# Performance work log

Hardware: AMD Instinct MI355X
Metric: run time of the kernel (lower is better)

The kernel has to match this reference:

```python
import jax, jax.numpy as jnp
import numpy as np

B, T_ENC, T_DEC = 64, 100, 50
L = 512      # lstm_size
E = 512      # input_encoding_size
H = 512      # att_hidden_size
R = 8        # num_review_steps
V_TOK = 30001  # token_cnt + 1 embedding rows
V_OUT = 30000  # word_cnt


def _lstm_maxout(s, c):
    # ARNet/neuraltalk2 LSTMCore: 5*L preactivations, maxout input transform
    i = jax.nn.sigmoid(s[:, :L])
    f = jax.nn.sigmoid(s[:, L:2 * L])
    o = jax.nn.sigmoid(s[:, 2 * L:3 * L])
    t = jnp.maximum(s[:, 3 * L:4 * L], s[:, 4 * L:])
    c2 = f * c + i * t
    return o * jnp.tanh(c2), c2


def _attend(feats, h, Wa2a, ba2a, Wh2a, bh2a, Watt, batt):
    # feats: [B, A, F], h: [B, L] -> context [B, F]
    p = jnp.tanh(feats @ Wa2a + ba2a + (h @ Wh2a + bh2a)[:, None, :])  # [B,A,H]
    e = jnp.squeeze(p @ Watt, -1) + batt                               # [B,A]
    a = jax.nn.softmax(e, axis=-1)
    return jnp.einsum('ba,baf->bf', a, feats)


def setup_inputs() -> dict:
    key = jax.random.key(0)
    ks = iter(jax.random.split(key, 48))
    g = lambda shape: jax.random.normal(next(ks), shape, jnp.float32) * 0.05
    z = lambda shape: jnp.zeros(shape, jnp.float32)
    return {
        'code_matrix': jax.random.randint(next(ks), (B, T_ENC), 0, V_TOK),
        'comment_matrix': jax.random.randint(next(ks), (B, T_DEC), 0, V_TOK),
        'current_comment_mask_cuda': jnp.ones((B, T_DEC), jnp.float32),
        'embed': jax.random.uniform(next(ks), (V_TOK, E), jnp.float32, -0.1, 0.1),
        'enc_Wi': g((E, 5 * L)), 'enc_bi': z((5 * L,)),
        'enc_Wh': g((L, 5 * L)), 'enc_bh': z((5 * L,)),
        'rev_Wh': g((R, L, 5 * L)), 'rev_bh': z((R, 5 * L)),
        'rev_Wa': g((R, L, 5 * L)), 'rev_ba': z((R, 5 * L)),
        'rev_Wa2a': g((R, L, H)), 'rev_ba2a': z((R, H)),
        'rev_Wh2a': g((R, L, H)), 'rev_bh2a': z((R, H)),
        'rev_Watt': g((R, H, 1)), 'rev_batt': z((R,)),
        'dec_Wi': g((E, 5 * L)), 'dec_bi': z((5 * L,)),
        'dec_Wh': g((L, 5 * L)), 'dec_bh': z((5 * L,)),
        'dec_Wa': g((L, 5 * L)), 'dec_ba': z((5 * L,)),
        'dec_Wa2a': g((L, H)), 'dec_ba2a': z((H,)),
        'dec_Wh2a': g((L, H)), 'dec_bh2a': z((H,)),
        'dec_Watt': g((H, 1)), 'dec_batt': z(()),
        'logit_W': jax.random.uniform(next(ks), (L, V_OUT), jnp.float32, -0.1, 0.1),
        'logit_b': z((V_OUT,)),
    }


def reference(code_matrix, comment_matrix, current_comment_mask_cuda, embed,
              enc_Wi, enc_bi, enc_Wh, enc_bh,
              rev_Wh, rev_bh, rev_Wa, rev_ba, rev_Wa2a, rev_ba2a,
              rev_Wh2a, rev_bh2a, rev_Watt, rev_batt,
              dec_Wi, dec_bi, dec_Wh, dec_bh, dec_Wa, dec_ba,
              dec_Wa2a, dec_ba2a, dec_Wh2a, dec_bh2a, dec_Watt, dec_batt,
              logit_W, logit_b):
    del current_comment_mask_cuda  # only used by scheduled sampling (ss_prob=0)
    Bsz = code_matrix.shape[0]
    h0 = jnp.zeros((Bsz, L), embed.dtype)
    c0 = jnp.zeros((Bsz, L), embed.dtype)

    # ---- encode ----
    enc_x = embed[code_matrix]  # [B, T_enc, E]

    def enc_step(carry, xt):
        h, c = carry
        s = xt @ enc_Wi + enc_bi + h @ enc_Wh + enc_bh
        h2, c2 = _lstm_maxout(s, c)
        return (h2, c2), h2

    (h_enc, c_enc), enc_hs = jax.lax.scan(enc_step, (h0, c0), jnp.swapaxes(enc_x, 0, 1))
    enc_hs = jnp.swapaxes(enc_hs, 0, 1)  # [B, T_enc, L]

    # ---- review (distinct params per step; scan over stacked params) ----
    def rev_step(carry, p):
        h, c = carry
        Wh, bh, Wa, ba, Wa2a, ba2a, Wh2a, bh2a, Watt, batt = p
        att_v = _attend(enc_hs, h, Wa2a, ba2a, Wh2a, bh2a, Watt, batt)
        s = h @ Wh + bh + att_v @ Wa + ba
        h2, c2 = _lstm_maxout(s, c)
        return (h2, c2), h2

    rev_params = (rev_Wh, rev_bh, rev_Wa, rev_ba, rev_Wa2a, rev_ba2a,
                  rev_Wh2a, rev_bh2a, rev_Watt, rev_batt)
    _, thought = jax.lax.scan(rev_step, (h_enc, c_enc), rev_params)
    thought = jnp.swapaxes(thought, 0, 1)  # [B, R, L]

    # ---- decode (teacher forcing; decode_state starts from encode_state) ----
    dec_x = embed[comment_matrix]  # [B, T_dec, E]

    def dec_step(carry, xt):
        h, c = carry
        att_v = _attend(thought, h, dec_Wa2a, dec_ba2a, dec_Wh2a, dec_bh2a, dec_Watt, dec_batt)
        s = xt @ dec_Wi + dec_bi + h @ dec_Wh + dec_bh + att_v @ dec_Wa + dec_ba
        h2, c2 = _lstm_maxout(s, c)
        logp = jax.nn.log_softmax(h2 @ logit_W + logit_b, axis=-1)
        return (h2, c2), logp

    _, logps = jax.lax.scan(dec_step, (h_enc, c_enc), jnp.swapaxes(dec_x, 0, 1))
    return jnp.swapaxes(logps, 0, 1)  # [B, T_dec, V_OUT]
```

## Files before the change

kernel.cpp:

```cpp
#include <hip/hip_runtime.h>
#include <math.h>
#include <stdint.h>

#define BB     64
#define TENC   100
#define TDEC   50
#define LDIM   512
#define EE     512
#define HDIM   512
#define FIVEL  2560
#define RSTEPS 8
#define VOUT   30000
#define NB2    470

typedef __attribute__((ext_vector_type(8))) short short8v;
typedef __attribute__((ext_vector_type(4))) float floatx4;
typedef unsigned short ushort_t;

static const size_t OFF_A        = 0;
static const size_t OFF_WIT_ENC  = 8192000;
static const size_t OFF_ENCX     = 8847360;
static const size_t OFF_LOGWT    = 0;
static const size_t OFF_DECH     = 7680000;
static const size_t OFF_DECPRE   = 8499200;
static const size_t OFF_ENC_HS   = 13107200;
static const size_t OFF_TPW      = 13107200;
static const size_t OFF_ENC_WHT  = 14745600;
static const size_t OFF_REVWC    = 15400960;
static const size_t OFF_PART     = 15400960;
static const size_t OFF_DECWC    = 25886720;
static const size_t OFF_WIT_DEC  = 27197440;
static const size_t OFF_REVWT    = 27852800;
static const size_t OFF_DECWT    = 28901376;
static const size_t OFF_REVWH2AT = 29032448;
static const size_t OFF_DECWH2AT = 30081024;
static const size_t OFF_DECX     = 30212096;
static const size_t OFF_THOUGHT  = 31031296;
static const size_t OFF_TPROJ    = 31162368;
static const size_t OFF_HB0      = 31293440;
static const size_t OFF_HB1      = 31309824;
static const size_t OFF_ATTV     = 31326208;
static const size_t OFF_H0       = 31342592;
static const size_t OFF_C0       = 31358976;
static const size_t OFF_SBUF     = 31490048;
static const size_t OFF_ALPHA    = 31653888;
static const size_t WS_TOTAL     = 31654400;

__device__ __forceinline__ float sigmoidf_(float x) { return 1.0f / (1.0f + __expf(-x)); }
__device__ __forceinline__ float tanh_fast(float x) { return 1.0f - 2.0f / (__expf(2.0f * x) + 1.0f); }
__device__ __forceinline__ unsigned short f2bf(float x) {
    unsigned u = __float_as_uint(x);
    u += 0x7FFFu + ((u >> 16) & 1u);
    return (unsigned short)(u >> 16);
}
__device__ __forceinline__ float bf2f(unsigned short h) {
    return __uint_as_float(((unsigned)h) << 16);
}

__global__ __launch_bounds__(128)
void gather_embed(const float* __restrict__ embed, const int* __restrict__ tok,
                  int T, ushort_t* __restrict__ X)
{
    int m = blockIdx.x, t = m / BB, b = m % BB;
    const float* src = embed + (size_t)tok[b * T + t] * EE;
    float4 v = *(const float4*)(src + threadIdx.x * 4);
    ushort4 o = { f2bf(v.x), f2bf(v.y), f2bf(v.z), f2bf(v.w) };
    *(ushort4*)(X + (size_t)m * EE + threadIdx.x * 4) = o;
}

__global__ __launch_bounds__(256)
void conv_transpose(const float* __restrict__ W, ushort_t* __restrict__ WT,
                    int N, int ldWT, int kofs, long Wz, long WTz)
{
    W  += (size_t)blockIdx.z * Wz;
    WT += (size_t)blockIdx.z * WTz;
    __shared__ float tile[32][33];
    int n0 = blockIdx.x * 32, k0 = blockIdx.y * 32;
    int tx = threadIdx.x & 31, ty = threadIdx.x >> 5;
    #pragma unroll
    for (int i = 0; i < 4; ++i) {
        int k = k0 + ty + i * 8, n = n0 + tx;
        tile[ty + i * 8][tx] = (n < N) ? W[(size_t)k * N + n] : 0.f;
    }
    __syncthreads();
    #pragma unroll
    for (int i = 0; i < 4; ++i) {
        int n = n0 + ty + i * 8, k = k0 + tx;
        if (n < N) WT[(size_t)n * ldWT + kofs + k] = f2bf(tile[tx][ty + i * 8]);
    }
}

__global__ __launch_bounds__(256)
void gemm_bf16(const ushort_t* __restrict__ A, const ushort_t* __restrict__ BT,
               const float* __restrict__ bias, ushort_t* __restrict__ Cb,
               int N, int K, long ldc)
{
    __shared__ ushort_t lds[2][128][32];
    __shared__ ushort_t ctile[128 * 128];
    const int tid  = threadIdx.x;
    const int wave = tid >> 6, lane = tid & 63;
    const int m0 = blockIdx.y * 128, n0 = blockIdx.x * 128;
    const int wr = wave >> 1, wc = wave & 1;

    floatx4 acc[4][4] = {};
    const int sr  = lane >> 2;
    const int scp = lane & 3;

    for (int k0 = 0; k0 < K; k0 += 32) {
        #pragma unroll
        for (int half = 0; half < 2; ++half) {
            int rbase = wave * 32 + half * 16;
            int r = rbase + sr;
            int c = scp ^ ((r >> 1) & 3);
            const ushort_t* ga = A + (size_t)(m0 + r) * K + k0 + c * 8;
            const ushort_t* gb = BT + (size_t)(n0 + r) * K + k0 + c * 8;
            __builtin_amdgcn_global_load_lds(
                (const __attribute__((address_space(1))) void*)ga,
                (__attribute__((address_space(3))) void*)&lds[0][rbase][0], 16, 0, 0);
            __builtin_amdgcn_global_load_lds(
                (const __attribute__((address_space(1))) void*)gb,
                (__attribute__((address_space(3))) void*)&lds[1][rbase][0], 16, 0, 0);
        }
        __syncthreads();

        short8v af[4], bv[4];
        #pragma unroll
        for (int i = 0; i < 4; ++i) {
            int ra = wr * 64 + i * 16 + (lane & 15);
            int ca = (lane >> 4) ^ ((ra >> 1) & 3);
            af[i] = *(const short8v*)&lds[0][ra][ca * 8];
            int rb = wc * 64 + i * 16 + (lane & 15);
            int cb = (lane >> 4) ^ ((rb >> 1) & 3);
            bv[i] = *(const short8v*)&lds[1][rb][cb * 8];
        }
        #pragma unroll
        for (int i = 0; i < 4; ++i)
            #pragma unroll
            for (int j = 0; j < 4; ++j)
                acc[i][j] = __builtin_amdgcn_mfma_f32_16x16x32_bf16(af[i], bv[j], acc[i][j], 0, 0, 0);
        __syncthreads();
    }

    const int crow0 = wr * 64 + (lane >> 4) * 4;
    const int ccol0 = wc * 64 + (lane & 15);
    #pragma unroll
    for (int i = 0; i < 4; ++i) {
        #pragma unroll
        for (int j = 0; j < 4; ++j) {
            int col = ccol0 + j * 16;
            float bval = bias ? bias[n0 + col] : 0.f;
            #pragma unroll
            for (int rr = 0; rr < 4; ++rr)
                ctile[(crow0 + i * 16 + rr) * 128 + col] = f2bf(acc[i][j][rr] + bval);
        }
    }
    __syncthreads();
    #pragma unroll
    for (int itc = 0; itc < 8; ++itc) {
        int chunk = itc * 256 + tid;
        int row = chunk >> 4, ch = chunk & 15;
        *(short8v*)(Cb + (size_t)(m0 + row) * ldc + n0 + ch * 8) =
            *(const short8v*)&ctile[row * 128 + ch * 8];
    }
}

__global__ __launch_bounds__(256)
void gemm_logit(const ushort_t* __restrict__ A, const ushort_t* __restrict__ BT,
                const float* __restrict__ bias, float* __restrict__ C,
                float2* __restrict__ part, int N, int K)
{
    __shared__ ushort_t lds[2][128][32];
    __shared__ float ctf[128 * 128];
    const int tid  = threadIdx.x;
    const int wave = tid >> 6, lane = tid & 63;
    int lin = blockIdx.x;
    int xcd = lin & 7, o = lin >> 3;
    int wgid = (xcd < 3 ? xcd * 735 + o : 3 * 735 + (xcd - 3) * 734 + o);
    const int ntile = wgid / 25, mtile = wgid % 25;
    const int m0 = mtile * 128, n0 = ntile * 128;
    const int wr = wave >> 1, wc = wave & 1;

    floatx4 acc[4][4] = {};
    const int sr  = lane >> 2;
    const int scp = lane & 3;

    for (int k0 = 0; k0 < K; k0 += 32) {
        #pragma unroll
        for (int half = 0; half < 2; ++half) {
            int rbase = wave * 32 + half * 16;
            int r = rbase + sr;
            int c = scp ^ ((r >> 1) & 3);
            const ushort_t* ga = A + (size_t)(m0 + r) * K + k0 + c * 8;
            int nr = n0 + r; if (nr >= N) nr = 0;
            const ushort_t* gb = BT + (size_t)nr * K + k0 + c * 8;
            __builtin_amdgcn_global_load_lds(
                (const __attribute__((address_space(1))) void*)ga,
                (__attribute__((address_space(3))) void*)&lds[0][rbase][0], 16, 0, 0);
            __builtin_amdgcn_global_load_lds(
                (const __attribute__((address_space(1))) void*)gb,
                (__attribute__((address_space(3))) void*)&lds[1][rbase][0], 16, 0, 0);
        }
        __syncthreads();

        short8v af[4], bv[4];
        #pragma unroll
        for (int i = 0; i < 4; ++i) {
            int ra = wr * 64 + i * 16 + (lane & 15);
            int ca = (lane >> 4) ^ ((ra >> 1) & 3);
            af[i] = *(const short8v*)&lds[0][ra][ca * 8];
            int rb = wc * 64 + i * 16 + (lane & 15);
            int cb = (lane >> 4) ^ ((rb >> 1) & 3);
            bv[i] = *(const short8v*)&lds[1][rb][cb * 8];
        }
        #pragma unroll
        for (int i = 0; i < 4; ++i)
            #pragma unroll
            for (int j = 0; j < 4; ++j)
                acc[i][j] = __builtin_amdgcn_mfma_f32_16x16x32_bf16(af[i], bv[j], acc[i][j], 0, 0, 0);
        __syncthreads();
    }

    const int cn = lane & 15, qq = lane >> 4;
    const int lcol0 = wc * 64 + cn;
    float bv[4]; bool valid[4];
    #pragma unroll
    for (int j = 0; j < 4; ++j) {
        int col = n0 + lcol0 + j * 16;
        valid[j] = col < N;
        bv[j] = valid[j] ? bias[col] : 0.f;
    }
    const int nb2 = ntile * 2 + wc;
    #pragma unroll
    for (int i = 0; i < 4; ++i) {
        #pragma unroll
        for (int rr = 0; rr < 4; ++rr) {
            int lrow = wr * 64 + qq * 4 + i * 16 + rr;
            int m = m0 + lrow;
            float v[4];
            #pragma unroll
            for (int j = 0; j < 4; ++j)
                v[j] = valid[j] ? acc[i][j][rr] + bv[j] : -3.0e38f;
            float mx = fmaxf(fmaxf(v[0], v[1]), fmaxf(v[2], v[3]));
            #pragma unroll
            for (int msk = 1; msk < 16; msk <<= 1) mx = fmaxf(mx, __shfl_xor(mx, msk));
            float sm = 0.f;
            #pragma unroll
            for (int j = 0; j < 4; ++j) if (valid[j]) sm += __expf(v[j] - mx);
            #pragma unroll
            for (int msk = 1; msk < 16; msk <<= 1) sm += __shfl_xor(sm, msk);
            if (cn == 0) part[(size_t)m * NB2 + nb2] = make_float2(mx, sm);
            #pragma unroll
            for (int j = 0; j < 4; ++j)
                ctf[lrow * 128 + lcol0 + j * 16] = v[j];
        }
    }
    __syncthreads();
    #pragma unroll
    for (int itc = 0; itc < 16; ++itc) {
        int chunk = itc * 256 + tid;
        int row = chunk >> 5, ch = chunk & 31;
        int col = n0 + ch * 4;
        if (col < N) {
            int m = m0 + row;
            int t = m >> 6, bb = m & 63;
            float* dst = C + ((size_t)bb * TDEC + t) * VOUT + col;
            if (col + 3 < N) {
                *(floatx4*)dst = *(const floatx4*)&ctf[row * 128 + ch * 4];
            } else {
                for (int e = 0; e < 4 && col + e < N; ++e)
                    dst[e] = ctf[row * 128 + ch * 4 + e];
            }
        }
    }
}

__global__ __launch_bounds__(256)
void logsm_sub(float* __restrict__ out, const float2* __restrict__ part)
{
    const int r = blockIdx.x;
    const int b = r / TDEC, t = r % TDEC;
    const int m = t * 64 + b;
    const int tid = threadIdx.x, wave = tid >> 6, lane = tid & 63;
    float M = -3.0e38f, S = 0.f;
    for (int i = tid; i < NB2; i += 256) {
        float2 p = part[(size_t)m * NB2 + i];
        float nm = fmaxf(M, p.x);
        S = S * __expf(M - nm) + p.y * __expf(p.x - nm);
        M = nm;
    }
    #pragma unroll
    for (int off = 32; off; off >>= 1) {
        float Mo = __shfl_xor(M, off), So = __shfl_xor(S, off);
        float nm = fmaxf(M, Mo);
        S = S * __expf(M - nm) + So * __expf(Mo - nm);
        M = nm;
    }
    __shared__ float ms[4], ss[4];
    if (lane == 0) { ms[wave] = M; ss[wave] = S; }
    __syncthreads();
    float M2 = fmaxf(fmaxf(ms[0], ms[1]), fmaxf(ms[2], ms[3]));
    float S2 = ss[0] * __expf(ms[0] - M2) + ss[1] * __expf(ms[1] - M2) +
               ss[2] * __expf(ms[2] - M2) + ss[3] * __expf(ms[3] - M2);
    float lse = M2 + __logf(S2);
    floatx4* row = (floatx4*)(out + (size_t)r * VOUT);
    for (int i = tid; i < VOUT / 4; i += 256) {
        floatx4 x = __builtin_nontemporal_load(row + i);
        x[0] -= lse; x[1] -= lse; x[2] -= lse; x[3] -= lse;
        __builtin_nontemporal_store(x, row + i);
    }
}

template<int NSEG>
__global__ __launch_bounds__(256)
void step_gemm(const ushort_t* __restrict__ a0, const ushort_t* __restrict__ a1,
               const ushort_t* __restrict__ BT, int ldBT, float* __restrict__ sbuf)
{
    constexpr int K = NSEG * 512;
    constexpr int LROW = K + 8;
    __shared__ ushort_t Bl[16 * LROW];
    const int tid = threadIdx.x, wave = tid >> 6, lane = tid & 63;
    const int q = lane >> 4, cn = lane & 15;
    const int n0 = blockIdx.x * 16;

    #pragma unroll
    for (int it = 0; it < NSEG * 4; ++it) {
        int slot = it * 4 + wave;
        int row  = slot / NSEG;
        int part = slot % NSEG;
        const ushort_t* src = BT + (size_t)(n0 + row) * ldBT + part * 512 + lane * 8;
        __builtin_amdgcn_global_load_lds(
            (const __attribute__((address_space(1))) void*)src,
            (__attribute__((address_space(3))) void*)&Bl[row * LROW + part * 512], 16, 0, 0);
    }
    __syncthreads();

    floatx4 acc = {0.f, 0.f, 0.f, 0.f};
    {
        const ushort_t* Ap = a0 + (size_t)(wave * 16 + cn) * 512 + q * 8;
        #pragma unroll
        for (int kt = 0; kt < 16; ++kt) {
            short8v af = *(const short8v*)(Ap + kt * 32);
            short8v bf = *(const short8v*)&Bl[cn * LROW + kt * 32 + q * 8];
            acc = __builtin_amdgcn_mfma_f32_16x16x32_bf16(af, bf, acc, 0, 0, 0);
        }
    }
    if (NSEG == 2) {
        const ushort_t* Ap = a1 + (size_t)(wave * 16 + cn) * 512 + q * 8;
        #pragma unroll
        for (int kt = 0; kt < 16; ++kt) {
            short8v af = *(const short8v*)(Ap + kt * 32);
            short8v bf = *(const short8v*)&Bl[cn * LROW + 512 + kt * 32 + q * 8];
            acc = __builtin_amdgcn_mfma_f32_16x16x32_bf16(af, bf, acc, 0, 0, 0);
        }
    }
    #pragma unroll
    for (int rr = 0; rr < 4; ++rr)
        sbuf[(size_t)(wave * 16 + q * 4 + rr) * FIVEL + n0 + cn] = acc[rr];
}

__global__ __launch_bounds__(256)
void lstm_epi(const float* __restrict__ s, const ushort_t* __restrict__ pre,
              const float* __restrict__ b0, const float* __restrict__ b1,
              const float* __restrict__ c_in, float* __restrict__ c_out,
              ushort_t* __restrict__ h_out, ushort_t* __restrict__ h_copy)
{
    int idx = blockIdx.x * 256 + threadIdx.x;
    int row = idx >> 8;
    int c   = (idx & 255) * 2;
    float sg[5][2];
    #pragma unroll
    for (int g = 0; g < 5; ++g) {
        float2 v = *(const float2*)(s + (size_t)row * FIVEL + g * 512 + c);
        sg[g][0] = v.x + b0[g * 512 + c];
        sg[g][1] = v.y + b0[g * 512 + c + 1];
        if (b1) {
            sg[g][0] += b1[g * 512 + c];
            sg[g][1] += b1[g * 512 + c + 1];
        }
        if (pre) {
            ushort2 p = *(const ushort2*)(pre + (size_t)row * FIVEL + g * 512 + c);
            sg[g][0] += bf2f(p.x);
            sg[g][1] += bf2f(p.y);
        }
    }
    float2 ci = *(const float2*)(c_in + (size_t)row * 512 + c);
    float cc[2] = {ci.x, ci.y};
    ushort_t hh[2];
    #pragma unroll
    for (int e = 0; e < 2; ++e) {
        float ig = sigmoidf_(sg[0][e]), fg = sigmoidf_(sg[1][e]), og = sigmoidf_(sg[2][e]);
        float tt = fmaxf(sg[3][e], sg[4][e]);
        float c2 = fg * cc[e] + ig * tt;
        cc[e] = c2;
        hh[e] = f2bf(og * tanh_fast(c2));
    }
    *(float2*)(c_out + (size_t)row * 512 + c) = make_float2(cc[0], cc[1]);
    ushort2 ho = {hh[0], hh[1]};
    *(ushort2*)(h_out + (size_t)row * 512 + c) = ho;
    if (h_copy) *(ushort2*)(h_copy + (size_t)row * 512 + c) = ho;
}

__global__ __launch_bounds__(256)
void epi_att(const float* __restrict__ s, const ushort_t* __restrict__ hprev,
             const ushort_t* __restrict__ pre,
             const float* __restrict__ b0, const float* __restrict__ b1,
             const ushort_t* __restrict__ tpw, const float* __restrict__ alpha_in,
             const float* __restrict__ c_in, float* __restrict__ c_out,
             ushort_t* __restrict__ h_out, ushort_t* __restrict__ h_copy,
             const ushort_t* __restrict__ projBase, long projLd,
             const ushort_t* __restrict__ feats,
             const ushort_t* __restrict__ W2aT, const float* __restrict__ b2a,
             const float* __restrict__ Watt,
             ushort_t* __restrict__ attv_out, float* __restrict__ alphas_out, int A)
{
    __shared__ ushort_t hl[512];
    __shared__ float hp[512];
    __shared__ float ealpha[128];
    const int b = blockIdx.x;
    const int tid = threadIdx.x, wave = tid >> 6, lane = tid & 63;

    if (s) {
        const int c = tid * 2;
        float al[8];
        if (tpw) {
            #pragma unroll
            for (int a = 0; a < 8; ++a) al[a] = alpha_in[b * 8 + a];
        }
        float sg[5][2];
        #pragma unroll
        for (int g = 0; g < 5; ++g) {
            float2 v = *(const float2*)(s + (size_t)b * FIVEL + g * 512 + c);
            sg[g][0] = v.x + b0[g * 512 + c];
            sg[g][1] = v.y + b0[g * 512 + c + 1];
            if (b1) {
                sg[g][0] += b1[g * 512 + c];
                sg[g][1] += b1[g * 512 + c + 1];
            }
            if (pre) {
                ushort2 p = *(const ushort2*)(pre + (size_t)b * FIVEL + g * 512 + c);
                sg[g][0] += bf2f(p.x);
                sg[g][1] += bf2f(p.y);
            }
            if (tpw) {
                #pragma unroll
                for (int a = 0; a < 8; ++a) {
                    ushort2 tv = *(const ushort2*)(tpw + ((size_t)a * 64 + b) * FIVEL + g * 512 + c);
                    sg[g][0] += al[a] * bf2f(tv.x);
                    sg[g][1] += al[a] * bf2f(tv.y);
                }
            }
        }
        float2 ci = *(const float2*)(c_in + (size_t)b * 512 + c);
        float cc[2] = {ci.x, ci.y};
        ushort_t hh[2];
        #pragma unroll
        for (int e = 0; e < 2; ++e) {
            float ig = sigmoidf_(sg[0][e]), fg = sigmoidf_(sg[1][e]), og = sigmoidf_(sg[2][e]);
            float tt = fmaxf(sg[3][e], sg[4][e]);
            float c2 = fg * cc[e] + ig * tt;
            cc[e] = c2;
            hh[e] = f2bf(og * tanh_fast(c2));
        }
        *(float2*)(c_out + (size_t)b * 512 + c) = make_float2(cc[0], cc[1]);
        ushort2 ho = {hh[0], hh[1]};
        *(ushort2*)(h_out + (size_t)b * 512 + c) = ho;
        if (h_copy) *(ushort2*)(h_copy + (size_t)b * 512 + c) = ho;
        *(ushort2*)&hl[c] = ho;
    } else {
        *(ushort2*)&hl[tid * 2] = *(const ushort2*)(hprev + (size_t)b * 512 + tid * 2);
    }
    if (!W2aT) return;
    __syncthreads();

    const int q = lane >> 4, cn = lane & 15;
    floatx4 acc[8] = {};
    {
        const ushort_t* Bp = W2aT + (size_t)(wave * 128 + cn) * 512 + q * 8;
        #pragma unroll 2
        for (int kt = 0; kt < 16; ++kt) {
            short8v af = *(const short8v*)&hl[kt * 32 + q * 8];
            #pragma unroll
            for (int t8 = 0; t8 < 8; ++t8) {
                short8v bf = *(const short8v*)(Bp + (size_t)t8 * 16 * 512 + kt * 32);
                acc[t8] = __builtin_amdgcn_mfma_f32_16x16x32_bf16(af, bf, acc[t8], 0, 0, 0);
            }
        }
    }
    if (q == 0) {
        #pragma unroll
        for (int t8 = 0; t8 < 8; ++t8) {
            int n = wave * 128 + t8 * 16 + cn;
            hp[n] = acc[t8][0] + b2a[n];
        }
    }
    __syncthreads();

    float hpr[8], war[8];
    {
        float4 w0 = *(const float4*)(Watt + lane * 8);
        float4 w1 = *(const float4*)(Watt + lane * 8 + 4);
        war[0] = w0.x; war[1] = w0.y; war[2] = w0.z; war[3] = w0.w;
        war[4] = w1.x; war[5] = w1.y; war[6] = w1.z; war[7] = w1.w;
        #pragma unroll
        for (int j = 0; j < 8; ++j) hpr[j] = hp[lane * 8 + j];
    }

    for (int a = wave; a < A; a += 4) {
        short8v pv = *(const short8v*)(projBase + ((size_t)a * 64 + b) * projLd + lane * 8);
        float e = 0.f;
        #pragma unroll
        for (int j = 0; j < 8; ++j)
            e += tanh_fast(bf2f((ushort_t)pv[j]) + hpr[j]) * war[j];
        #pragma unroll
        for (int off = 32; off; off >>= 1) e += __shfl_xor(e, off);
        if (lane == 0) ealpha[a] = e;
    }
    __syncthreads();
    if (wave == 0) {
        float v1 = (lane < A) ? ealpha[lane] : -3.0e38f;
        float v2 = (lane + 64 < A) ? ealpha[lane + 64] : -3.0e38f;
        float mm = fmaxf(v1, v2);
        #pragma unroll
        for (int off = 32; off; off >>= 1) mm = fmaxf(mm, __shfl_xor(mm, off));
        float x1 = (lane < A) ? __expf(v1 - mm) : 0.f;
        float x2 = (lane + 64 < A) ? __expf(v2 - mm) : 0.f;
        float ss = x1 + x2;
        #pragma unroll
        for (int off = 32; off; off >>= 1) ss += __shfl_xor(ss, off);
        float inv = 1.f / ss;
        if (lane < A) ealpha[lane] = x1 * inv;
        if (lane + 64 < A) ealpha[lane + 64] = x2 * inv;
    }
    __syncthreads();

    if (attv_out) {
        float s0 = 0.f, s1 = 0.f;
        for (int a = 0; a < A; ++a) {
            float alv = ealpha[a];
            unsigned int u = *(const unsigned int*)(feats + ((size_t)a * 64 + b) * 512 + tid * 2);
            s0 += alv * bf2f((ushort_t)(u & 0xffffu));
            s1 += alv * bf2f((ushort_t)(u >> 16));
        }
        ushort2 o = { f2bf(s0), f2bf(s1) };
        *(ushort2*)(attv_out + (size_t)b * 512 + tid * 2) = o;
    } else {
        if (tid < A) alphas_out[b * A + tid] = ealpha[tid];
    }
}

__global__ __launch_bounds__(256)
void attfuse2(const ushort_t* __restrict__ hprev,
              const ushort_t* __restrict__ projBase, long projLd,
              const ushort_t* __restrict__ feats,
              const ushort_t* __restrict__ W2aT, const float* __restrict__ b2a,
              const float* __restrict__ Watt, ushort_t* __restrict__ attv, int A)
{
    __shared__ float hp[512];
    __shared__ float ealpha[128];
    const int b = blockIdx.x;
    const int tid = threadIdx.x, wave = tid >> 6, lane = tid & 63;
    const int q = lane >> 4, cn = lane & 15;

    floatx4 acc[8] = {};
    {
        const ushort_t* Ap = hprev + (size_t)b * 512 + q * 8;
        const ushort_t* Bp = W2aT + (size_t)(wave * 128 + cn) * 512 + q * 8;
        #pragma unroll 2
        for (int kt = 0; kt < 16; ++kt) {
            short8v af = *(const short8v*)(Ap + kt * 32);
            #pragma unroll
            for (int t8 = 0; t8 < 8; ++t8) {
                short8v bf = *(const short8v*)(Bp + (size_t)t8 * 16 * 512 + kt * 32);
                acc[t8] = __builtin_amdgcn_mfma_f32_16x16x32_bf16(af, bf, acc[t8], 0, 0, 0);
            }
        }
    }
    if (q == 0) {
        #pragma unroll
        for (int t8 = 0; t8 < 8; ++t8) {
            int n = wave * 128 + t8 * 16 + cn;
            hp[n] = acc[t8][0] + b2a[n];
        }
    }
    __syncthreads();

    float hpr[8], war[8];
    {
        float4 w0 = *(const float4*)(Watt + lane * 8);
        float4 w1 = *(const float4*)(Watt + lane * 8 + 4);
        war[0] = w0.x; war[1] = w0.y; war[2] = w0.z; war[3] = w0.w;
        war[4] = w1.x; war[5] = w1.y; war[6] = w1.z; war[7] = w1.w;
        #pragma unroll
        for (int j = 0; j < 8; ++j) hpr[j] = hp[lane * 8 + j];
    }

    for (int a = wave; a < A; a += 4) {
        short8v pv = *(const short8v*)(projBase + ((size_t)a * 64 + b) * projLd + lane * 8);
        float e = 0.f;
        #pragma unroll
        for (int j = 0; j < 8; ++j)
            e += tanh_fast(bf2f((ushort_t)pv[j]) + hpr[j]) * war[j];
        #pragma unroll
        for (int off = 32; off; off >>= 1) e += __shfl_xor(e, off);
        if (lane == 0) ealpha[a] = e;
    }
    __syncthreads();
    if (wave == 0) {
        float v1 = (lane < A) ? ealpha[lane] : -3.0e38f;
        float v2 = (lane + 64 < A) ? ealpha[lane + 64] : -3.0e38f;
        float mm = fmaxf(v1, v2);
        #pragma unroll
        for (int off = 32; off; off >>= 1) mm = fmaxf(mm, __shfl_xor(mm, off));
        float x1 = (lane < A) ? __expf(v1 - mm) : 0.f;
        float x2 = (lane + 64 < A) ? __expf(v2 - mm) : 0.f;
        float ss = x1 + x2;
        #pragma unroll
        for (int off = 32; off; off >>= 1) ss += __shfl_xor(ss, off);
        float inv = 1.f / ss;
        if (lane < A) ealpha[lane] = x1 * inv;
        if (lane + 64 < A) ealpha[lane + 64] = x2 * inv;
    }
    __syncthreads();

    float s0 = 0.f, s1 = 0.f;
    for (int a = 0; a < A; ++a) {
        float al = ealpha[a];
        unsigned int u = *(const unsigned int*)(feats + ((size_t)a * 64 + b) * 512 + tid * 2);
        s0 += al * bf2f((ushort_t)(u & 0xffffu));
        s1 += al * bf2f((ushort_t)(u >> 16));
    }
    ushort2 o = { f2bf(s0), f2bf(s1) };
    *(ushort2*)(attv + (size_t)b * 512 + tid * 2) = o;
}

extern "C" void kernel_launch(void* const* d_in, const int* in_sizes, int n_in,
                              void* d_out_, int out_size, void* d_ws, size_t ws_size,
                              hipStream_t stream)
{
    const int*   code     = (const int*)  d_in[0];
    const int*   comment  = (const int*)  d_in[1];
    const float* embed    = (const float*)d_in[3];
    const float* enc_Wi   = (const float*)d_in[4];
    const float* enc_bi   = (const float*)d_in[5];
    const float* enc_Wh   = (const float*)d_in[6];
    const float* enc_bh   = (const float*)d_in[7];
    const float* rev_Wh   = (const float*)d_in[8];
    const float* rev_bh   = (const float*)d_in[9];
    const float* rev_Wa   = (const float*)d_in[10];
    const float* rev_ba   = (const float*)d_in[11];
    const float* rev_Wa2a = (const float*)d_in[12];
    const float* rev_ba2a = (const float*)d_in[13];
    const float* rev_Wh2a = (const float*)d_in[14];
    const float* rev_bh2a = (const float*)d_in[15];
    const float* rev_Watt = (const float*)d_in[16];
    const float* dec_Wi   = (const float*)d_in[18];
    const float* dec_bi   = (const float*)d_in[19];
    const float* dec_Wh   = (const float*)d_in[20];
    const float* dec_bh   = (const float*)d_in[21];
    const float* dec_Wa   = (const float*)d_in[22];
    const float* dec_ba   = (const float*)d_in[23];
    const float* dec_Wa2a = (const float*)d_in[24];
    const float* dec_ba2a = (const float*)d_in[25];
    const float* dec_Wh2a = (const float*)d_in[26];
    const float* dec_bh2a = (const float*)d_in[27];
    const float* dec_Watt = (const float*)d_in[28];
    const float* logit_W  = (const float*)d_in[30];
    const float* logit_b  = (const float*)d_in[31];
    float* out = (float*)d_out_;

    float* ws = (float*)d_ws;
    if (ws_size < WS_TOTAL * sizeof(float)) return;

    ushort_t* enc_pre_b = (ushort_t*)(ws + OFF_A);
    ushort_t* rev_projA = (ushort_t*)(ws + OFF_A);
    ushort_t* logit_WT  = (ushort_t*)(ws + OFF_LOGWT);
    ushort_t* dec_h_b   = (ushort_t*)(ws + OFF_DECH);
    ushort_t* dec_pre_b = (ushort_t*)(ws + OFF_DECPRE);
    ushort_t* WiT_enc   = (ushort_t*)(ws + OFF_WIT_ENC);
    ushort_t* enc_x_b   = (ushort_t*)(ws + OFF_ENCX);
    ushort_t* enc_hs_b  = (ushort_t*)(ws + OFF_ENC_HS);
    ushort_t* TPW       = (ushort_t*)(ws + OFF_TPW);
    ushort_t* encWhT    = (ushort_t*)(ws + OFF_ENC_WHT);
    ushort_t* revWcomb  = (ushort_t*)(ws + OFF_REVWC);
    float2*   part      = (float2*)(ws + OFF_PART);
    ushort_t* decWhT    = (ushort_t*)(ws + OFF_DECWC);
    ushort_t* WaT_dec   = (ushort_t*)(ws + OFF_DECWC + 655360);
    ushort_t* WiT_dec   = (ushort_t*)(ws + OFF_WIT_DEC);
    ushort_t* revWT     = (ushort_t*)(ws + OFF_REVWT);
    ushort_t* decWT     = (ushort_t*)(ws + OFF_DECWT);
    ushort_t* revWh2aT  = (ushort_t*)(ws + OFF_REVWH2AT);
    ushort_t* decWh2aT  = (ushort_t*)(ws + OFF_DECWH2AT);
    ushort_t* dec_x_b   = (ushort_t*)(ws + OFF_DECX);
    ushort_t* thought_b = (ushort_t*)(ws + OFF_THOUGHT);
    ushort_t* tproj_b   = (ushort_t*)(ws + OFF_TPROJ);
    ushort_t* hb[2] = { (ushort_t*)(ws + OFF_HB0), (ushort_t*)(ws + OFF_HB1) };
    ushort_t* attv_b    = (ushort_t*)(ws + OFF_ATTV);
    ushort_t* h0_b      = (ushort_t*)(ws + OFF_H0);
    float*    sbuf      = ws + OFF_SBUF;
    float*    alphas    = ws + OFF_ALPHA;
    float* cbuf[4];
    for (int i = 0; i < 4; ++i) cbuf[i] = ws + OFF_C0 + (size_t)i * 32768;

    const dim3 blk(256);

    (void)hipMemsetAsync(cbuf[0], 0, (size_t)BB * LDIM * sizeof(float), stream);
    (void)hipMemsetAsync(h0_b, 0, (size_t)BB * LDIM * sizeof(ushort_t), stream);

    gather_embed<<<TENC * BB, 128, 0, stream>>>(embed, code, TENC, enc_x_b);
    gather_embed<<<TDEC * BB, 128, 0, stream>>>(embed, comment, TDEC, dec_x_b);
    conv_transpose<<<dim3(80, 16, 1), blk, 0, stream>>>(enc_Wi, WiT_enc, FIVEL, 512, 0, 0, 0);
    conv_transpose<<<dim3(80, 16, 1), blk, 0, stream>>>(enc_Wh, encWhT, FIVEL, 512, 0, 0, 0);
    conv_transpose<<<dim3(80, 16, 8), blk, 0, stream>>>(rev_Wh, revWcomb, FIVEL, 1024, 0,   1310720, 2621440);
    conv_transpose<<<dim3(80, 16, 8), blk, 0, stream>>>(rev_Wa, revWcomb, FIVEL, 1024, 512, 1310720, 2621440);
    conv_transpose<<<dim3(16, 16, 8), blk, 0, stream>>>(rev_Wa2a, revWT, 512, 512, 0,       262144, 262144);
    conv_transpose<<<dim3(16, 16, 8), blk, 0, stream>>>(rev_Wh2a, revWh2aT, 512, 512, 0,    262144, 262144);
    conv_transpose<<<dim3(80, 16, 1), blk, 0, stream>>>(dec_Wi, WiT_dec, FIVEL, 512, 0, 0, 0);
    conv_transpose<<<dim3(80, 16, 1), blk, 0, stream>>>(dec_Wh, decWhT, FIVEL, 512, 0, 0, 0);
    conv_transpose<<<dim3(80, 16, 1), blk, 0, stream>>>(dec_Wa, WaT_dec, FIVEL, 512, 0, 0, 0);
    conv_transpose<<<dim3(16, 16, 1), blk, 0, stream>>>(dec_Wa2a, decWT, 512, 512, 0, 0, 0);
    conv_transpose<<<dim3(16, 16, 1), blk, 0, stream>>>(dec_Wh2a, decWh2aT, 512, 512, 0, 0, 0);

    gemm_bf16<<<dim3(FIVEL / 128, TENC * BB / 128), blk, 0, stream>>>(
        enc_x_b, WiT_enc, enc_bi, enc_pre_b, FIVEL, EE, FIVEL);

    for (int t = 0; t < TENC; ++t) {
        const ushort_t* hin = (t == 0) ? h0_b : enc_hs_b + (size_t)(t - 1) * 32768;
        step_gemm<1><<<160, blk, 0, stream>>>(hin, nullptr, encWhT, 512, sbuf);
        lstm_epi<<<64, blk, 0, stream>>>(
            sbuf, enc_pre_b + (size_t)t * 163840, enc_bh, nullptr,
            cbuf[t & 1], cbuf[(t + 1) & 1],
            enc_hs_b + (size_t)t * 32768, nullptr);
    }
    const ushort_t* h_enc = enc_hs_b + (size_t)(TENC - 1) * 32768;

    gemm_bf16<<<dim3(32, 50), blk, 0, stream>>>(
        enc_hs_b, revWT, rev_ba2a, rev_projA, 4096, LDIM, 4096);

    attfuse2<<<BB, blk, 0, stream>>>(
        h_enc, rev_projA, 4096, enc_hs_b,
        revWh2aT, rev_bh2a, rev_Watt, attv_b, TENC);
    const ushort_t* rh = h_enc;
    for (int r = 0; r < RSTEPS; ++r) {
        step_gemm<2><<<160, blk, 0, stream>>>(
            rh, attv_b, revWcomb + (size_t)r * 2621440, 1024, sbuf);
        const float* ci = (r == 0) ? cbuf[0] : cbuf[2 + ((r - 1) & 1)];
        const ushort_t* nextW = (r < RSTEPS - 1) ? revWh2aT + (size_t)(r + 1) * 262144 : nullptr;
        epi_att<<<BB, blk, 0, stream>>>(
            sbuf, nullptr, nullptr,
            rev_bh + (size_t)r * FIVEL, rev_ba + (size_t)r * FIVEL,
            nullptr, nullptr,
            ci, cbuf[2 + (r & 1)],
            hb[r & 1], thought_b + (size_t)r * 32768,
            rev_projA + (size_t)(r + 1) * 512, 4096, enc_hs_b,
            nextW, rev_bh2a + (size_t)(r + 1) * 512, rev_Watt + (size_t)(r + 1) * 512,
            attv_b, nullptr, TENC);
        rh = hb[r & 1];
    }

    gemm_bf16<<<dim3(4, 4), blk, 0, stream>>>(
        thought_b, decWT, dec_ba2a, tproj_b, HDIM, LDIM, HDIM);
    conv_transpose<<<dim3((VOUT + 31) / 32, 16, 1), blk, 0, stream>>>(
        logit_W, logit_WT, VOUT, 512, 0, 0, 0);
    gemm_bf16<<<dim3(FIVEL / 128, TDEC * BB / 128), blk, 0, stream>>>(
        dec_x_b, WiT_dec, dec_bi, dec_pre_b, FIVEL, EE, FIVEL);
    gemm_bf16<<<dim3(20, 4), blk, 0, stream>>>(
        thought_b, WaT_dec, nullptr, TPW, FIVEL, LDIM, FIVEL);

    epi_att<<<BB, blk, 0, stream>>>(
        nullptr, h_enc, nullptr, nullptr, nullptr, nullptr, nullptr,
        nullptr, nullptr, nullptr, nullptr,
        tproj_b, 512, nullptr,
        decWh2aT, dec_bh2a, dec_Watt, nullptr, alphas, RSTEPS);
    for (int t = 0; t < TDEC; ++t) {
        const ushort_t* dh = (t == 0) ? h_enc : hb[(t - 1) & 1];
        step_gemm<1><<<160, blk, 0, stream>>>(dh, nullptr, decWhT, 512, sbuf);
        const float* ci = (t == 0) ? cbuf[0] : cbuf[2 + ((t - 1) & 1)];
        const ushort_t* nextW = (t < TDEC - 1) ? decWh2aT : nullptr;
        epi_att<<<BB, blk, 0, stream>>>(
            sbuf, nullptr, dec_pre_b + (size_t)t * 163840,
            dec_bh, dec_ba,
            TPW, alphas,
            ci, cbuf[2 + (t & 1)],
            hb[t & 1], dec_h_b + (size_t)t * 32768,
            tproj_b, 512, nullptr,
            nextW, dec_bh2a, dec_Watt, nullptr, alphas, RSTEPS);
    }

    gemm_logit<<<dim3(235 * 25), blk, 0, stream>>>(
        dec_h_b, logit_WT, logit_b, out, part, VOUT, LDIM);
    logsm_sub<<<TDEC * BB, blk, 0, stream>>>(out, part);
}
```

Before: 3.351 ms.

## Fuse encoder LSTM epilogue into next step's recurrent GEMM and batch weight transposes

The encoder loop drops the separate step_gemm and lstm_epi launches per timestep. One fused kernel now has every block recompute the full LSTM epilogue for all 64 rows into LDS, then run its 32-column slice of h@Wh with MFMA. Results ping-pong between two s buffers, and the first step skips the zero-h GEMM. The eleven weight-transpose launches are merged into four z-indexed kernels. This halves the encoder's per-step launches and round trips, at the cost of redundant elementwise epilogue work across 80 blocks.

New measurement: 6.426 ms. 1.92x slower.

```diff
diff --git a/kernel.cpp b/kernel.cpp
--- a/kernel.cpp
+++ b/kernel.cpp
@@ -16,6 +16,9 @@
 typedef __attribute__((ext_vector_type(8))) short short8v;
 typedef __attribute__((ext_vector_type(4))) float floatx4;
 typedef unsigned short ushort_t;
+
+#define AS1 __attribute__((address_space(1)))
+#define AS3 __attribute__((address_space(3)))
 
 static const size_t OFF_A        = 0;
 static const size_t OFF_WIT_ENC  = 8192000;
@@ -43,8 +46,9 @@
 static const size_t OFF_H0       = 31342592;
 static const size_t OFF_C0       = 31358976;
 static const size_t OFF_SBUF     = 31490048;
-static const size_t OFF_ALPHA    = 31653888;
-static const size_t WS_TOTAL     = 31654400;
+static const size_t OFF_SBUF1    = 31653888;
+static const size_t OFF_ALPHA    = 31817728;
+static const size_t WS_TOTAL     = 31818240;
 
 __device__ __forceinline__ float sigmoidf_(float x) { return 1.0f / (1.0f + __expf(-x)); }
 __device__ __forceinline__ float tanh_fast(float x) { return 1.0f - 2.0f / (__expf(2.0f * x) + 1.0f); }
@@ -68,12 +72,10 @@
     *(ushort4*)(X + (size_t)m * EE + threadIdx.x * 4) = o;
 }
 
-__global__ __launch_bounds__(256)
-void conv_transpose(const float* __restrict__ W, ushort_t* __restrict__ WT,
-                    int N, int ldWT, int kofs, long Wz, long WTz)
-{
-    W  += (size_t)blockIdx.z * Wz;
-    WT += (size_t)blockIdx.z * WTz;
+__device__ __forceinline__ void transpose_body(const float* __restrict__ W,
+                                               ushort_t* __restrict__ WT,
+                                               int N, int ldWT, int kofs)
+{
     __shared__ float tile[32][33];
     int n0 = blockIdx.x * 32, k0 = blockIdx.y * 32;
     int tx = threadIdx.x & 31, ty = threadIdx.x >> 5;
@@ -88,6 +90,53 @@
         int n = n0 + ty + i * 8, k = k0 + tx;
         if (n < N) WT[(size_t)n * ldWT + kofs + k] = f2bf(tile[tx][ty + i * 8]);
     }
+}
+
+__global__ __launch_bounds__(256)
+void conv_transpose(const float* __restrict__ W, ushort_t* __restrict__ WT,
+                    int N, int ldWT, int kofs)
+{
+    transpose_body(W, WT, N, ldWT, kofs);
+}
+
+__global__ __launch_bounds__(256)
+void conv_transpose5(const float* W0, const float* W1, const float* W2,
+                     const float* W3, const float* W4,
+                     ushort_t* D0, ushort_t* D1, ushort_t* D2,
+                     ushort_t* D3, ushort_t* D4)
+{
+    const float* W; ushort_t* D;
+    switch (blockIdx.z) {
+        case 0:  W = W0; D = D0; break;
+        case 1:  W = W1; D = D1; break;
+        case 2:  W = W2; D = D2; break;
+        case 3:  W = W3; D = D3; break;
+        default: W = W4; D = D4; break;
+    }
+    transpose_body(W, D, FIVEL, 512, 0);
+}
+
+__global__ __launch_bounds__(256)
+void conv_transpose_rev(const float* __restrict__ Wh, const float* __restrict__ Wa,
+                        ushort_t* __restrict__ WT)
+{
+    int zz = blockIdx.z;
+    int r = zz & 7;
+    const float* W = (zz < 8 ? Wh : Wa) + (size_t)r * 1310720;
+    ushort_t* D = WT + (size_t)r * 2621440;
+    transpose_body(W, D, FIVEL, 1024, (zz < 8) ? 0 : 512);
+}
+
+__global__ __launch_bounds__(256)
+void conv_transpose_sq(const float* __restrict__ A0, const float* __restrict__ A1,
+                       ushort_t* __restrict__ D0, ushort_t* __restrict__ D1,
+                       int zsplit, long Wz, long WTz)
+{
+    int zz = blockIdx.z;
+    const float* W; ushort_t* D;
+    if (zz < zsplit) { W = A0 + (size_t)zz * Wz; D = D0 + (size_t)zz * WTz; }
+    else             { W = A1 + (size_t)(zz - zsplit) * Wz; D = D1 + (size_t)(zz - zsplit) * WTz; }
+    transpose_body(W, D, 512, 512, 0);
 }
 
 __global__ __launch_bounds__(256)
@@ -115,11 +164,9 @@
             const ushort_t* ga = A + (size_t)(m0 + r) * K + k0 + c * 8;
             const ushort_t* gb = BT + (size_t)(n0 + r) * K + k0 + c * 8;
             __builtin_amdgcn_global_load_lds(
-                (const __attribute__((address_space(1))) void*)ga,
-                (__attribute__((address_space(3))) void*)&lds[0][rbase][0], 16, 0, 0);
+                (const AS1 void*)ga, (AS3 void*)&lds[0][rbase][0], 16, 0, 0);
             __builtin_amdgcn_global_load_lds(
-                (const __attribute__((address_space(1))) void*)gb,
-                (__attribute__((address_space(3))) void*)&lds[1][rbase][0], 16, 0, 0);
+                (const AS1 void*)gb, (AS3 void*)&lds[1][rbase][0], 16, 0, 0);
         }
         __syncthreads();
 
@@ -194,11 +241,9 @@
             int nr = n0 + r; if (nr >= N) nr = 0;
             const ushort_t* gb = BT + (size_t)nr * K + k0 + c * 8;
             __builtin_amdgcn_global_load_lds(
-                (const __attribute__((address_space(1))) void*)ga,
-                (__attribute__((address_space(3))) void*)&lds[0][rbase][0], 16, 0, 0);
+                (const AS1 void*)ga, (AS3 void*)&lds[0][rbase][0], 16, 0, 0);
             __builtin_amdgcn_global_load_lds(
-                (const __attribute__((address_space(1))) void*)gb,
-                (__attribute__((address_space(3))) void*)&lds[1][rbase][0], 16, 0, 0);
+                (const AS1 void*)gb, (AS3 void*)&lds[1][rbase][0], 16, 0, 0);
         }
         __syncthreads();
 
@@ -310,6 +355,90 @@
     }
 }
 
+__global__ __launch_bounds__(256)
+void enc_step_fused(const float* __restrict__ sprev,
+                    const ushort_t* __restrict__ pre,
+                    const float* __restrict__ bh,
+                    const float* __restrict__ c_in, float* __restrict__ c_out,
+                    ushort_t* __restrict__ h_store,
+                    const ushort_t* __restrict__ WhT,
+                    float* __restrict__ sout)
+{
+    __shared__ ushort_t hl[64][520];
+    __shared__ ushort_t Bl[32][520];
+    const int tid = threadIdx.x, wave = tid >> 6, lane = tid & 63;
+    const int n0 = blockIdx.x * 32;
+
+    for (int r = wave; r < 32; r += 4) {
+        const ushort_t* src = WhT + (size_t)(n0 + r) * 512 + lane * 8;
+        __builtin_amdgcn_global_load_lds(
+            (const AS1 void*)src, (AS3 void*)&Bl[r][0], 16, 0, 0);
+    }
+
+    const int col4 = (tid & 127) * 4;
+    const int r0 = (tid >> 7) * 32;
+    float b0[5][4];
+    #pragma unroll
+    for (int g = 0; g < 5; ++g)
+        *(floatx4*)b0[g] = *(const floatx4*)(bh + g * 512 + col4);
+    const bool writerBlk = blockIdx.x < 8;
+    const int wrow0 = blockIdx.x * 8;
+
+    #pragma unroll 4
+    for (int rr = 0; rr < 32; ++rr) {
+        int row = r0 + rr;
+        float sg[5][4];
+        #pragma unroll
+        for (int g = 0; g < 5; ++g) {
+            floatx4 sv;
+            if (sprev) sv = *(const floatx4*)(sprev + (size_t)row * FIVEL + g * 512 + col4);
+            else       sv = (floatx4){0.f, 0.f, 0.f, 0.f};
+            ushort4 p = *(const ushort4*)(pre + (size_t)row * FIVEL + g * 512 + col4);
+            sg[g][0] = sv[0] + bf2f(p.x) + b0[g][0];
+            sg[g][1] = sv[1] + bf2f(p.y) + b0[g][1];
+            sg[g][2] = sv[2] + bf2f(p.z) + b0[g][2];
+            sg[g][3] = sv[3] + bf2f(p.w) + b0[g][3];
+        }
+        floatx4 ci = *(const floatx4*)(c_in + (size_t)row * 512 + col4);
+        floatx4 co;
+        ushort4 ho;
+        unsigned short hv[4];
+        #pragma unroll
+        for (int e = 0; e < 4; ++e) {
+            float ig = sigmoidf_(sg[0][e]), fg = sigmoidf_(sg[1][e]), og = sigmoidf_(sg[2][e]);
+            float tt = fmaxf(sg[3][e], sg[4][e]);
+            float c2 = fg * ci[e] + ig * tt;
+            co[e] = c2;
+            hv[e] = f2bf(og * tanh_fast(c2));
+        }
+        ho = make_ushort4(hv[0], hv[1], hv[2], hv[3]);
+        *(ushort4*)&hl[row][col4] = ho;
+        if (writerBlk && row >= wrow0 && row < wrow0 + 8) {
+            *(floatx4*)(c_out + (size_t)row * 512 + col4) = co;
+            *(ushort4*)(h_store + (size_t)row * 512 + col4) = ho;
+        }
+    }
+    __syncthreads();
+
+    const int q = lane >> 4, cn = lane & 15;
+    const int arow = wave * 16 + cn;
+    floatx4 acc[2] = {};
+    #pragma unroll
+    for (int kt = 0; kt < 16; ++kt) {
+        short8v af = *(const short8v*)&hl[arow][kt * 32 + q * 8];
+        #pragma unroll
+        for (int tl = 0; tl < 2; ++tl) {
+            short8v bf = *(const short8v*)&Bl[tl * 16 + cn][kt * 32 + q * 8];
+            acc[tl] = __builtin_amdgcn_mfma_f32_16x16x32_bf16(af, bf, acc[tl], 0, 0, 0);
+        }
+    }
+    #pragma unroll
+    for (int tl = 0; tl < 2; ++tl)
+        #pragma unroll
+        for (int rr = 0; rr < 4; ++rr)
+            sout[(size_t)(wave * 16 + q * 4 + rr) * FIVEL + n0 + tl * 16 + cn] = acc[tl][rr];
+}
+
 template<int NSEG>
 __global__ __launch_bounds__(256)
 void step_gemm(const ushort_t* __restrict__ a0, const ushort_t* __restrict__ a1,
@@ -329,8 +458,7 @@
         int part = slot % NSEG;
         const ushort_t* src = BT + (size_t)(n0 + row) * ldBT + part * 512 + lane * 8;
         __builtin_amdgcn_global_load_lds(
-            (const __attribute__((address_space(1))) void*)src,
-            (__attribute__((address_space(3))) void*)&Bl[row * LROW + part * 512], 16, 0, 0);
+            (const AS1 void*)src, (AS3 void*)&Bl[row * LROW + part * 512], 16, 0, 0);
     }
     __syncthreads();
 
@@ -695,8 +823,7 @@
     ushort_t* tproj_b   = (ushort_t*)(ws + OFF_TPROJ);
     ushort_t* hb[2] = { (ushort_t*)(ws + OFF_HB0), (ushort_t*)(ws + OFF_HB1) };
     ushort_t* attv_b    = (ushort_t*)(ws + OFF_ATTV);
-    ushort_t* h0_b      = (ushort_t*)(ws + OFF_H0);
-    float*    sbuf      = ws + OFF_SBUF;
+    float*    sb[2]     = { ws + OFF_SBUF, ws + OFF_SBUF1 };
     float*    alphas    = ws + OFF_ALPHA;
     float* cbuf[4];
     for (int i = 0; i < 4; ++i) cbuf[i] = ws + OFF_C0 + (size_t)i * 32768;
@@ -704,33 +831,36 @@
     const dim3 blk(256);
 
     (void)hipMemsetAsync(cbuf[0], 0, (size_t)BB * LDIM * sizeof(float), stream);
-    (void)hipMemsetAsync(h0_b, 0, (size_t)BB * LDIM * sizeof(ushort_t), stream);
 
     gather_embed<<<TENC * BB, 128, 0, stream>>>(embed, code, TENC, enc_x_b);
     gather_embed<<<TDEC * BB, 128, 0, stream>>>(embed, comment, TDEC, dec_x_b);
-    conv_transpose<<<dim3(80, 16, 1), blk, 0, stream>>>(enc_Wi, WiT_enc, FIVEL, 512, 0, 0, 0);
-    conv_transpose<<<dim3(80, 16, 1), blk, 0, stream>>>(enc_Wh, encWhT, FIVEL, 512, 0, 0, 0);
-    conv_transpose<<<dim3(80, 16, 8), blk, 0, stream>>>(rev_Wh, revWcomb, FIVEL, 1024, 0,   1310720, 2621440);
-    conv_transpose<<<dim3(80, 16, 8), blk, 0, stream>>>(rev_Wa, revWcomb, FIVEL, 1024, 512, 1310720, 2621440);
-    conv_transpose<<<dim3(16, 16, 8), blk, 0, stream>>>(rev_Wa2a, revWT, 512, 512, 0,       262144, 262144);
-    conv_transpose<<<dim3(16, 16, 8), blk, 0, stream>>>(rev_Wh2a, revWh2aT, 512, 512, 0,    262144, 262144);
-    conv_transpose<<<dim3(80, 16, 1), blk, 0, stream>>>(dec_Wi, WiT_dec, FIVEL, 512, 0, 0, 0);
-    conv_transpose<<<dim3(80, 16, 1), blk, 0, stream>>>(dec_Wh, decWhT, FIVEL, 512, 0, 0, 0);
-    conv_transpose<<<dim3(80, 16, 1), blk, 0, stream>>>(dec_Wa, WaT_dec, FIVEL, 512, 0, 0, 0);
-    conv_transpose<<<dim3(16, 16, 1), blk, 0, stream>>>(dec_Wa2a, decWT, 512, 512, 0, 0, 0);
-    conv_transpose<<<dim3(16, 16, 1), blk, 0, stream>>>(dec_Wh2a, decWh2aT, 512, 512, 0, 0, 0);
+    conv_transpose5<<<dim3(80, 16, 5), blk, 0, stream>>>(
+        enc_Wi, enc_Wh, dec_Wi, dec_Wh, dec_Wa,
+        WiT_enc, encWhT, WiT_dec, decWhT, WaT_dec);
+    conv_transpose_rev<<<dim3(80, 16, 16), blk, 0, stream>>>(rev_Wh, rev_Wa, revWcomb);
+    conv_transpose_sq<<<dim3(16, 16, 16), blk, 0, stream>>>(
+        rev_Wa2a, rev_Wh2a, revWT, revWh2aT, 8, 262144, 262144);
+    conv_transpose_sq<<<dim3(16, 16, 2), blk, 0, stream>>>(
+        dec_Wa2a, dec_Wh2a, decWT, decWh2aT, 1, 0, 0);
 
     gemm_bf16<<<dim3(FIVEL / 128, TENC * BB / 128), blk, 0, stream>>>(
         enc_x_b, WiT_enc, enc_bi, enc_pre_b, FIVEL, EE, FIVEL);
 
-    for (int t = 0; t < TENC; ++t) {
-        const ushort_t* hin = (t == 0) ? h0_b : enc_hs_b + (size_t)(t - 1) * 32768;
-        step_gemm<1><<<160, blk, 0, stream>>>(hin, nullptr, encWhT, 512, sbuf);
-        lstm_epi<<<64, blk, 0, stream>>>(
-            sbuf, enc_pre_b + (size_t)t * 163840, enc_bh, nullptr,
-            cbuf[t & 1], cbuf[(t + 1) & 1],
-            enc_hs_b + (size_t)t * 32768, nullptr);
-    }
+    for (int t = 1; t < TENC; ++t) {
+        enc_step_fused<<<80, blk, 0, stream>>>(
+            (t == 1) ? nullptr : sb[(t - 1) & 1],
+            enc_pre_b + (size_t)(t - 1) * 163840,
+            enc_bh,
+            (t == 1) ? cbuf[0] : cbuf[2 + ((t - 2) & 1)],
+            cbuf[2 + ((t - 1) & 1)],
+            enc_hs_b + (size_t)(t - 1) * 32768,
+            encWhT,
+            sb[t & 1]);
+    }
+    lstm_epi<<<64, blk, 0, stream>>>(
+        sb[(TENC - 1) & 1], enc_pre_b + (size_t)(TENC - 1) * 163840, enc_bh, nullptr,
+        cbuf[2 + ((TENC - 2) & 1)], cbuf[0],
+        enc_hs_b + (size_t)(TENC - 1) * 32768, nullptr);
     const ushort_t* h_enc = enc_hs_b + (size_t)(TENC - 1) * 32768;
 
     gemm_bf16<<<dim3(32, 50), blk, 0, stream>>>(
@@ -742,11 +872,11 @@
     const ushort_t* rh = h_enc;
     for (int r = 0; r < RSTEPS; ++r) {
         step_gemm<2><<<160, blk, 0, stream>>>(
-            rh, attv_b, revWcomb + (size_t)r * 2621440, 1024, sbuf);
+            rh, attv_b, revWcomb + (size_t)r * 2621440, 1024, sb[0]);
         const float* ci = (r == 0) ? cbuf[0] : cbuf[2 + ((r - 1) & 1)];
         const ushort_t* nextW = (r < RSTEPS - 1) ? revWh2aT + (size_t)(r + 1) * 262144 : nullptr;
         epi_att<<<BB, blk, 0, stream>>>(
-            sbuf, nullptr, nullptr,
+            sb[0], nullptr, nullptr,
             rev_bh + (size_t)r * FIVEL, rev_ba + (size_t)r * FIVEL,
             nullptr, nullptr,
             ci, cbuf[2 + (r & 1)],
@@ -760,7 +890,7 @@
     gemm_bf16<<<dim3(4, 4), blk, 0, stream>>>(
         thought_b, decWT, dec_ba2a, tproj_b, HDIM, LDIM, HDIM);
     conv_transpose<<<dim3((VOUT + 31) / 32, 16, 1), blk, 0, stream>>>(
-        logit_W, logit_WT, VOUT, 512, 0, 0, 0);
+        logit_W, logit_WT, VOUT, 512, 0);
     gemm_bf16<<<dim3(FIVEL / 128, TDEC * BB / 128), blk, 0, stream>>>(
         dec_x_b, WiT_dec, dec_bi, dec_pre_b, FIVEL, EE, FIVEL);
     gemm_bf16<<<dim3(20, 4), blk, 0, stream>>>(
@@ -773,11 +903,11 @@
         decWh2aT, dec_bh2a, dec_Watt, nullptr, alphas, RSTEPS);
     for (int t = 0; t < TDEC; ++t) {
         const ushort_t* dh = (t == 0) ? h_enc : hb[(t - 1) & 1];
-        step_gemm<1><<<160, blk, 0, stream>>>(dh, nullptr, decWhT, 512, sbuf);
+        step_gemm<1><<<160, blk, 0, stream>>>(dh, nullptr, decWhT, 512, sb[0]);
         const float* ci = (t == 0) ? cbuf[0] : cbuf[2 + ((t - 1) & 1)];
         const ushort_t* nextW = (t < TDEC - 1) ? decWh2aT : nullptr;
         epi_att<<<BB, blk, 0, stream>>>(
-            sbuf, nullptr, dec_pre_b + (size_t)t * 163840,
+            sb[0], nullptr, dec_pre_b + (size_t)t * 163840,
             dec_bh, dec_ba,
             TPW, alphas,
             ci, cbuf[2 + (t & 1)],
```
